# Kernel tuning notes

Hardware: AMD Instinct MI355X
Metric: run time of the kernel (lower is better)

The kernel has to match this reference:

```python
import jax, jax.numpy as jnp
import numpy as np

GROUPS = [21, 6, 17, 14, 20]
N = 78          # total nodes per graph
B = 8192        # batched graphs (original module processes one at a time)
RATIO = 0.2
LN_EPS = 1e-5


def _build_edges():
    """Replicates Graph_test mode='random' edge construction (incl. its offset quirk)."""
    rng = np.random.RandomState(0)
    edges = []
    offset = 0
    for num in GROUPS:
        for i in range(num):
            for j in range(num):
                if i != j:
                    edges.append((i + offset, j + offset))
        offset += num
    offset = 0
    for i in range(5):
        offset_2 = GROUPS[i]
        for j in range(i + 1, 5):
            for _i in range(GROUPS[i]):
                for _j in range(GROUPS[j]):
                    if _i + offset != _j + offset_2 and rng.random_sample() < RATIO:
                        edges.append((_i + offset, _j + offset_2))
            offset_2 += GROUPS[j]
        offset += GROUPS[i]
    return np.asarray(edges, dtype=np.int64).T  # [2, E]


def _ln(x, g, b):
    m = jnp.mean(x, axis=-1, keepdims=True)
    v = jnp.var(x, axis=-1, keepdims=True)
    return (x - m) * jax.lax.rsqrt(v + LN_EPS) * g + b


def _tconv(x, src, tgt, wq, bq, wk, bk, wv, bv, ws, bs, H, C):
    """PyG TransformerConv (concat=True, root_weight=True, no beta/edge_dim)."""
    n = x.shape[0]
    q = (x @ wq.T + bq).reshape(n, H, C)
    k = (x @ wk.T + bk).reshape(n, H, C)
    v = (x @ wv.T + bv).reshape(n, H, C)
    alpha = jnp.sum(q[tgt] * k[src], axis=-1) / np.sqrt(float(C))      # [E, H]
    amax = jax.ops.segment_max(alpha, tgt, num_segments=n)             # [N, H]
    e = jnp.exp(alpha - amax[tgt])
    den = jax.ops.segment_sum(e, tgt, num_segments=n)
    w = e / den[tgt]                                                   # softmax per target node
    out = jax.ops.segment_sum(w[..., None] * v[src], tgt, num_segments=n)
    return out.reshape(n, H * C) + (x @ ws.T + bs)                     # skip connection


def _forward(src, tgt, cli_data, radio_data, ln1_g, ln1_b, enc_w, enc_b,
             q1_w, q1_b, k1_w, k1_b, v1_w, v1_b, s1_w, s1_b,
             q2_w, q2_b, k2_w, k2_b, v2_w, v2_b, s2_w, s2_b,
             ln2_g, ln2_b, cls_w, cls_b):
    h = _ln(radio_data, ln1_g, ln1_b) @ enc_w.T + enc_b   # Linear(384,20)
    h = jax.nn.leaky_relu(h)                              # dropout = identity (eval)
    x = jnp.concatenate([cli_data, h], axis=1)[..., None]  # [B, 78, 1]

    def graph(xg):  # xg: [78, 1]
        y = jax.nn.leaky_relu(_tconv(xg, src, tgt, q1_w, q1_b, k1_w, k1_b,
                                     v1_w, v1_b, s1_w, s1_b, 4, 1))      # [78, 4]
        y = jax.nn.leaky_relu(_tconv(y, src, tgt, q2_w, q2_b, k2_w, k2_b,
                                     v2_w, v2_b, s2_w, s2_b, 1, 1))      # [78, 1]
        return y[:, 0]                                                    # [78]

    y = jax.vmap(graph)(x)                                # [B, 78]
    return _ln(y, ln2_g, ln2_b) @ cls_w.T + cls_b         # [B, 2]


def setup_inputs() -> dict:
    key = jax.random.key(0)
    ks = jax.random.split(key, 12)

    def xav(k, shape):
        lim = np.sqrt(6.0 / (shape[0] + shape[1]))
        return jax.random.uniform(k, shape, jnp.float32, -lim, lim)

    ei = jnp.asarray(_build_edges())
    return dict(
        cli_data=jax.random.normal(ks[0], (B, 58), jnp.float32),
        radio_data=jax.random.normal(ks[1], (B, 384), jnp.float32),
        edge_index=ei,
        ln1_g=jnp.ones((384,), jnp.float32), ln1_b=jnp.zeros((384,), jnp.float32),
        enc_w=xav(ks[2], (20, 384)), enc_b=jnp.zeros((20,), jnp.float32),
        q1_w=xav(ks[3], (4, 1)), q1_b=jnp.zeros((4,), jnp.float32),
        k1_w=xav(ks[4], (4, 1)), k1_b=jnp.zeros((4,), jnp.float32),
        v1_w=xav(ks[5], (4, 1)), v1_b=jnp.zeros((4,), jnp.float32),
        s1_w=xav(ks[6], (4, 1)), s1_b=jnp.zeros((4,), jnp.float32),
        q2_w=xav(ks[7], (1, 4)), q2_b=jnp.zeros((1,), jnp.float32),
        k2_w=xav(ks[8], (1, 4)), k2_b=jnp.zeros((1,), jnp.float32),
        v2_w=xav(ks[9], (1, 4)), v2_b=jnp.zeros((1,), jnp.float32),
        s2_w=xav(ks[10], (1, 4)), s2_b=jnp.zeros((1,), jnp.float32),
        ln2_g=jnp.ones((N,), jnp.float32), ln2_b=jnp.zeros((N,), jnp.float32),
        cls_w=xav(ks[11], (2, N)), cls_b=jnp.zeros((2,), jnp.float32),
    )


def reference(cli_data, radio_data, edge_index, ln1_g, ln1_b, enc_w, enc_b,
              q1_w, q1_b, k1_w, k1_b, v1_w, v1_b, s1_w, s1_b,
              q2_w, q2_b, k2_w, k2_b, v2_w, v2_b, s2_w, s2_b,
              ln2_g, ln2_b, cls_w, cls_b):
    src, tgt = edge_index[0], edge_index[1]
    return _forward(src, tgt, cli_data, radio_data, ln1_g, ln1_b, enc_w, enc_b,
                    q1_w, q1_b, k1_w, k1_b, v1_w, v1_b, s1_w, s1_b,
                    q2_w, q2_b, k2_w, k2_b, v2_w, v2_b, s2_w, s2_b,
                    ln2_g, ln2_b, cls_w, cls_b)


if __name__ == '__main__':
    out = reference(**setup_inputs())
    print(out.shape)
```

## Files before the change

### kernel.cpp

```cpp
#include <hip/hip_runtime.h>

#define LREL(x) ((x) > 0.0f ? (x) : 0.01f * (x))
#define LOG2E 1.44269504f

constexpr int NNODE = 78;
constexpr int GPB   = 16;
constexpr int ROWS  = 32;
constexpr int BLOCK = GPB * ROWS;
constexpr int NI    = 3;
constexpr int PADS  = 17;

__global__ void build_csr_kernel(const int* __restrict__ ei, int E,
                                 int* __restrict__ row_ptr,
                                 int* __restrict__ csr_src,
                                 int* __restrict__ perm) {
    __shared__ int cnt[NNODE];
    __shared__ int cur[NNODE];
    __shared__ int deg[NNODE];
    int tid = threadIdx.x;
    if (tid < NNODE) cnt[tid] = 0;
    __syncthreads();
    for (int e = tid; e < E; e += blockDim.x)
        atomicAdd(&cnt[ei[E + e]], 1);
    __syncthreads();
    if (tid < NNODE) deg[tid] = cnt[tid];
    __syncthreads();
    if (tid == 0) {
        int acc = 0;
        for (int n = 0; n < NNODE; ++n) {
            row_ptr[n] = acc;
            cur[n]     = acc;
            acc += cnt[n];
        }
        row_ptr[NNODE] = acc;
    }
    if (tid < NNODE) {
        int d = deg[tid], rank = 0;
        for (int m = 0; m < NNODE; ++m) {
            int dm = deg[m];
            rank += (dm > d) || (dm == d && m < tid);
        }
        perm[rank] = tid;
    }
    if (tid >= NNODE && tid < ROWS * NI) perm[tid] = -1;
    __syncthreads();
    for (int e = tid; e < E; e += blockDim.x) {
        int t   = ei[E + e];
        int pos = atomicAdd(&cur[t], 1);
        csr_src[pos] = ei[e] * PADS;
    }
}

__global__ __launch_bounds__(256) void encode_kernel(
    const float* __restrict__ radio,
    const float* __restrict__ ln1g, const float* __restrict__ ln1b,
    const float* __restrict__ encw, const float* __restrict__ encb,
    int Bn, float* __restrict__ hout) {

    const int tid  = threadIdx.x;
    const int w    = tid >> 6;
    const int half = (tid >> 5) & 1;
    const int l32  = tid & 31;

    const float4* radio4 = (const float4*)radio;
    const float4* encw4  = (const float4*)encw;
    const float4* g14    = (const float4*)ln1g;
    const float4* b14    = (const float4*)ln1b;

    float4 xn0[3], xn1[3];
    const long g0 = (long)blockIdx.x * 16 + w * 4 + half;
    const long g1 = g0 + 2;

#pragma unroll
    for (int pp = 0; pp < 2; ++pp) {
        long gidx = pp ? g1 : g0;
        bool ok = gidx < Bn;
        float4* xn = pp ? xn1 : xn0;
        float s = 0.0f, q = 0.0f;
#pragma unroll
        for (int i = 0; i < 3; ++i) {
            float4 v = ok ? radio4[gidx * 96 + l32 + 32 * i]
                          : make_float4(0, 0, 0, 0);
            xn[i] = v;
            s += v.x + v.y + v.z + v.w;
            q += v.x * v.x + v.y * v.y + v.z * v.z + v.w * v.w;
        }
#pragma unroll
        for (int o = 16; o; o >>= 1) {
            s += __shfl_xor(s, o, 32);
            q += __shfl_xor(q, o, 32);
        }
        float mean = s * (1.0f / 384.0f);
        float var  = q * (1.0f / 384.0f) - mean * mean;
        float rstd = rsqrtf(var + 1e-5f);
#pragma unroll
        for (int i = 0; i < 3; ++i) {
            float4 gv = g14[l32 + 32 * i];
            float4 bv = b14[l32 + 32 * i];
            float4 v  = xn[i];
            v.x = (v.x - mean) * rstd * gv.x + bv.x;
            v.y = (v.y - mean) * rstd * gv.y + bv.y;
            v.z = (v.z - mean) * rstd * gv.z + bv.z;
            v.w = (v.w - mean) * rstd * gv.w + bv.w;
            xn[i] = v;
        }
    }

    float h0 = 0.0f, h1 = 0.0f;
    for (int j = 0; j < 20; ++j) {
        float4 w0 = encw4[j * 96 + l32];
        float4 w1 = encw4[j * 96 + l32 + 32];
        float4 w2 = encw4[j * 96 + l32 + 64];
#pragma unroll
        for (int pp = 0; pp < 2; ++pp) {
            const float4* xn = pp ? xn1 : xn0;
            float p = xn[0].x * w0.x;
            p = fmaf(xn[0].y, w0.y, p); p = fmaf(xn[0].z, w0.z, p);
            p = fmaf(xn[0].w, w0.w, p);
            p = fmaf(xn[1].x, w1.x, p); p = fmaf(xn[1].y, w1.y, p);
            p = fmaf(xn[1].z, w1.z, p); p = fmaf(xn[1].w, w1.w, p);
            p = fmaf(xn[2].x, w2.x, p); p = fmaf(xn[2].y, w2.y, p);
            p = fmaf(xn[2].w, w2.w, p); p = fmaf(xn[2].z, w2.z, p);
#pragma unroll
            for (int o = 16; o; o >>= 1) p += __shfl_xor(p, o, 32);
            if (pp) h1 = (l32 == j) ? p : h1;
            else    h0 = (l32 == j) ? p : h0;
        }
    }
    if (l32 < 20) {
        float eb = encb[l32];
        if (g0 < Bn) hout[g0 * 20 + l32] = LREL(h0 + eb);
        if (g1 < Bn) hout[g1 * 20 + l32] = LREL(h1 + eb);
    }
}

__global__ __launch_bounds__(BLOCK, 4) void graph_conv_kernel(
    const float* __restrict__ cli, const float* __restrict__ hin,
    const float* __restrict__ q1w, const float* __restrict__ q1b,
    const float* __restrict__ k1w, const float* __restrict__ k1b,
    const float* __restrict__ v1w, const float* __restrict__ v1b,
    const float* __restrict__ s1w, const float* __restrict__ s1b,
    const float* __restrict__ q2w, const float* __restrict__ q2b,
    const float* __restrict__ k2w, const float* __restrict__ k2b,
    const float* __restrict__ v2w, const float* __restrict__ v2b,
    const float* __restrict__ s2w, const float* __restrict__ s2b,
    const float* __restrict__ ln2g, const float* __restrict__ ln2b,
    const float* __restrict__ clsw, const float* __restrict__ clsb,
    const int* __restrict__ row_ptr, const int* __restrict__ csr_src,
    const int* __restrict__ perm,
    int E, int Bn, float* __restrict__ out) {

    __shared__ float s_feat[NNODE * PADS];
    __shared__ float s_k2[NNODE * PADS];
    __shared__ float s_v2[NNODE * PADS];
    __shared__ float s_redA[8 * PADS];
    __shared__ float s_redB[8 * PADS];
    __shared__ float s_statM[GPB];
    __shared__ float s_statR[GPB];
    __shared__ int   s_rp[NNODE + 1];
    __shared__ int   s_slot[ROWS * NI];
    extern __shared__ int s_csr[];

    const int tid  = threadIdx.x;
    const int g    = tid & 15;
    const int r    = tid >> 4;
    const int w    = tid >> 6;
    const int lane = tid & 63;
    const long base = (long)blockIdx.x * GPB;

    for (int i = tid; i < E; i += BLOCK) s_csr[i] = csr_src[i];
    if (tid < NNODE + 1) s_rp[tid] = row_ptr[tid];
    if (tid < ROWS * NI) s_slot[tid] = perm[tid];
    for (int idx = tid; idx < GPB * 58; idx += BLOCK) {
        int gg = idx / 58, c = idx - gg * 58;
        if (base + gg < Bn) s_feat[c * PADS + gg] = cli[(base + gg) * 58 + c];
    }
    if (tid < GPB * 20) {
        int gg = tid / 20, j = tid - gg * 20;
        if (base + gg < Bn) s_feat[(58 + j) * PADS + gg] = hin[(base + gg) * 20 + j];
    }

    const float Q1W0 = q1w[0], Q1W1 = q1w[1], Q1W2 = q1w[2], Q1W3 = q1w[3];
    const float Q1B0 = q1b[0], Q1B1 = q1b[1], Q1B2 = q1b[2], Q1B3 = q1b[3];
    const float K1L0 = k1w[0] * LOG2E, K1L1 = k1w[1] * LOG2E;
    const float K1L2 = k1w[2] * LOG2E, K1L3 = k1w[3] * LOG2E;
    const float V1W0 = v1w[0], V1W1 = v1w[1], V1W2 = v1w[2], V1W3 = v1w[3];
    const float V1B0 = v1b[0], V1B1 = v1b[1], V1B2 = v1b[2], V1B3 = v1b[3];
    const float S1W0 = s1w[0], S1W1 = s1w[1], S1W2 = s1w[2], S1W3 = s1w[3];
    const float S1B0 = s1b[0], S1B1 = s1b[1], S1B2 = s1b[2], S1B3 = s1b[3];
    const float Q2W0 = q2w[0], Q2W1 = q2w[1], Q2W2 = q2w[2], Q2W3 = q2w[3];
    const float K2W0 = k2w[0], K2W1 = k2w[1], K2W2 = k2w[2], K2W3 = k2w[3];
    const float V2W0 = v2w[0], V2W1 = v2w[1], V2W2 = v2w[2], V2W3 = v2w[3];
    const float S2W0 = s2w[0], S2W1 = s2w[1], S2W2 = s2w[2], S2W3 = s2w[3];
    const float Q2B = q2b[0], K2B = k2b[0], V2B = v2b[0], S2B = s2b[0];
    __syncthreads();

    int   nodes[NI];
    float y_q[NI], y_sk[NI], z[NI];

#pragma unroll
    for (int k = 0; k < NI; ++k) {
        int n = s_slot[k * ROWS + r];
        nodes[k] = n;
        bool act = n >= 0;
        int nn = act ? n : 0;
        float xv = s_feat[nn * PADS + g];
        float qh0 = fmaf(xv, Q1W0, Q1B0), qh1 = fmaf(xv, Q1W1, Q1B1);
        float qh2 = fmaf(xv, Q1W2, Q1B2), qh3 = fmaf(xv, Q1W3, Q1B3);
        float qa0 = qh0 * K1L0, qa1 = qh1 * K1L1;
        float qa2 = qh2 * K1L2, qa3 = qh3 * K1L3;
        float den0 = 0, den1 = 0, den2 = 0, den3 = 0;
        float wa0 = 0, wa1 = 0, wa2 = 0, wa3 = 0;
        int beg = s_rp[nn];
        int end = act ? s_rp[nn + 1] : beg;
        int i = beg;
        for (; i + 1 < end; i += 2) {
            int c0 = s_csr[i], c1 = s_csr[i + 1];
            float t0 = s_feat[c0 + g];
            float t1 = s_feat[c1 + g];
            float ea0 = exp2f(qa0 * t0), eb0 = exp2f(qa0 * t1);
            float ea1 = exp2f(qa1 * t0), eb1 = exp2f(qa1 * t1);
            float ea2 = exp2f(qa2 * t0), eb2 = exp2f(qa2 * t1);
            float ea3 = exp2f(qa3 * t0), eb3 = exp2f(qa3 * t1);
            den0 += ea0 + eb0; den1 += ea1 + eb1;
            den2 += ea2 + eb2; den3 += ea3 + eb3;
            wa0 = fmaf(ea0, t0, fmaf(eb0, t1, wa0));
            wa1 = fmaf(ea1, t0, fmaf(eb1, t1, wa1));
            wa2 = fmaf(ea2, t0, fmaf(eb2, t1, wa2));
            wa3 = fmaf(ea3, t0, fmaf(eb3, t1, wa3));
        }
        if (i < end) {
            int c0 = s_csr[i];
            float t0 = s_feat[c0 + g];
            float ea0 = exp2f(qa0 * t0), ea1 = exp2f(qa1 * t0);
            float ea2 = exp2f(qa2 * t0), ea3 = exp2f(qa3 * t0);
            den0 += ea0; den1 += ea1; den2 += ea2; den3 += ea3;
            wa0 = fmaf(ea0, t0, wa0); wa1 = fmaf(ea1, t0, wa1);
            wa2 = fmaf(ea2, t0, wa2); wa3 = fmaf(ea3, t0, wa3);
        }
        float y0 = LREL(fmaf(V1W0, wa0 / den0, V1B0) + fmaf(xv, S1W0, S1B0));
        float y1 = LREL(fmaf(V1W1, wa1 / den1, V1B1) + fmaf(xv, S1W1, S1B1));
        float y2 = LREL(fmaf(V1W2, wa2 / den2, V1B2) + fmaf(xv, S1W2, S1B2));
        float y3 = LREL(fmaf(V1W3, wa3 / den3, V1B3) + fmaf(xv, S1W3, S1B3));
        y_q[k]  = Q2B + y0 * Q2W0 + y1 * Q2W1 + y2 * Q2W2 + y3 * Q2W3;
        y_sk[k] = S2B + y0 * S2W0 + y1 * S2W1 + y2 * S2W2 + y3 * S2W3;
        if (act) {
            s_k2[n * PADS + g] = K2B + y0 * K2W0 + y1 * K2W1 + y2 * K2W2 + y3 * K2W3;
            s_v2[n * PADS + g] = V2B + y0 * V2W0 + y1 * V2W1 + y2 * V2W2 + y3 * V2W3;
        }
    }
    __syncthreads();

    float zs = 0, zq = 0;
#pragma unroll
    for (int k = 0; k < NI; ++k) {
        int n = nodes[k];
        bool act = n >= 0;
        int nn = act ? n : 0;
        float q = y_q[k];
        int beg = s_rp[nn];
        int end = act ? s_rp[nn + 1] : beg;
        float m = -1e30f;
        for (int i = beg; i < end; ++i)
            m = fmaxf(m, q * s_k2[s_csr[i] + g]);
        float ql = q * LOG2E, ml = m * LOG2E;
        float den = 0, acc = 0;
        int i = beg;
        for (; i + 1 < end; i += 2) {
            int c0 = s_csr[i], c1 = s_csr[i + 1];
            float k0 = s_k2[c0 + g], k1v = s_k2[c1 + g];
            float v0 = s_v2[c0 + g], v1v = s_v2[c1 + g];
            float e0 = exp2f(fmaf(ql, k0, -ml));
            float e1 = exp2f(fmaf(ql, k1v, -ml));
            den += e0 + e1;
            acc = fmaf(e0, v0, fmaf(e1, v1v, acc));
        }
        if (i < end) {
            int c0 = s_csr[i];
            float e0 = exp2f(fmaf(ql, s_k2[c0 + g], -ml));
            den += e0;
            acc = fmaf(e0, s_v2[c0 + g], acc);
        }
        float zz = LREL(acc / den + y_sk[k]);
        z[k] = zz;
        if (act) { zs += zz; zq = fmaf(zz, zz, zq); }
    }

    zs += __shfl_xor(zs, 16, 64); zs += __shfl_xor(zs, 32, 64);
    zq += __shfl_xor(zq, 16, 64); zq += __shfl_xor(zq, 32, 64);
    if (lane < 16) {
        s_redA[w * PADS + lane] = zs;
        s_redB[w * PADS + lane] = zq;
    }
    __syncthreads();
    if (tid < GPB) {
        float a = 0, bb = 0;
#pragma unroll
        for (int i = 0; i < 8; ++i) {
            a  += s_redA[i * PADS + tid];
            bb += s_redB[i * PADS + tid];
        }
        float mean = a * (1.0f / 78.0f);
        float var  = bb * (1.0f / 78.0f) - mean * mean;
        s_statM[tid] = mean;
        s_statR[tid] = rsqrtf(var + 1e-5f);
    }
    __syncthreads();
    float mean = s_statM[g], rstd = s_statR[g];
    float p0 = 0, p1 = 0;
#pragma unroll
    for (int k = 0; k < NI; ++k) {
        int n = nodes[k];
        if (n >= 0) {
            float zn = fmaf((z[k] - mean) * rstd, ln2g[n], ln2b[n]);
            p0 = fmaf(zn, clsw[n], p0);
            p1 = fmaf(zn, clsw[NNODE + n], p1);
        }
    }
    p0 += __shfl_xor(p0, 16, 64); p0 += __shfl_xor(p0, 32, 64);
    p1 += __shfl_xor(p1, 16, 64); p1 += __shfl_xor(p1, 32, 64);
    if (lane < 16) {
        s_redA[w * PADS + lane] = p0;
        s_redB[w * PADS + lane] = p1;
    }
    __syncthreads();
    if (tid < GPB) {
        float a = 0, bb = 0;
#pragma unroll
        for (int i = 0; i < 8; ++i) {
            a  += s_redA[i * PADS + tid];
            bb += s_redB[i * PADS + tid];
        }
        long gi = base + tid;
        if (gi < Bn) {
            out[gi * 2 + 0] = a + clsb[0];
            out[gi * 2 + 1] = bb + clsb[1];
        }
    }
}

extern "C" void kernel_launch(void* const* d_in, const int* in_sizes, int n_in,
                              void* d_out, int out_size, void* d_ws, size_t ws_size,
                              hipStream_t stream) {
    const float* cli   = (const float*)d_in[0];
    const float* radio = (const float*)d_in[1];
    const int*   ei    = (const int*)d_in[2];
    const float* ln1g = (const float*)d_in[3];
    const float* ln1b = (const float*)d_in[4];
    const float* encw = (const float*)d_in[5];
    const float* encb = (const float*)d_in[6];
    const float* q1w  = (const float*)d_in[7];
    const float* q1b  = (const float*)d_in[8];
    const float* k1w  = (const float*)d_in[9];
    const float* k1b  = (const float*)d_in[10];
    const float* v1w  = (const float*)d_in[11];
    const float* v1b  = (const float*)d_in[12];
    const float* s1w  = (const float*)d_in[13];
    const float* s1b  = (const float*)d_in[14];
    const float* q2w  = (const float*)d_in[15];
    const float* q2b  = (const float*)d_in[16];
    const float* k2w  = (const float*)d_in[17];
    const float* k2b  = (const float*)d_in[18];
    const float* v2w  = (const float*)d_in[19];
    const float* v2b  = (const float*)d_in[20];
    const float* s2w  = (const float*)d_in[21];
    const float* s2b  = (const float*)d_in[22];
    const float* ln2g = (const float*)d_in[23];
    const float* ln2b = (const float*)d_in[24];
    const float* clsw = (const float*)d_in[25];
    const float* clsb = (const float*)d_in[26];

    const int E  = in_sizes[2] / 2;
    const int Bn = in_sizes[0] / 58;

    int* row_ptr = (int*)d_ws;
    int* csr_src = row_ptr + 80;
    int* perm    = csr_src + E;
    int  off     = (80 + E + ROWS * NI + 7) & ~7;
    float* h     = (float*)((int*)d_ws + off);

    build_csr_kernel<<<1, 256, 0, stream>>>(ei, E, row_ptr, csr_src, perm);

    const int egrid = (Bn + 15) / 16;
    encode_kernel<<<egrid, 256, 0, stream>>>(radio, ln1g, ln1b, encw, encb, Bn, h);

    const int grid = (Bn + GPB - 1) / GPB;
    size_t shmem = (size_t)E * sizeof(int);
    graph_conv_kernel<<<grid, BLOCK, shmem, stream>>>(
        cli, h,
        q1w, q1b, k1w, k1b, v1w, v1b, s1w, s1b,
        q2w, q2b, k2w, k2b, v2w, v2b, s2w, s2b,
        ln2g, ln2b, clsw, clsb,
        row_ptr, csr_src, perm, E, Bn, (float*)d_out);
}
```

Measured before the change: 165.2 us.

## Halve graphs per block, double rows per graph, and compress CSR indices to 16-bit

The graph-conv kernel now handles 8 graphs per 512-thread block instead of 16. Each node-row thread processes at most 2 nodes instead of 3. The CSR, row pointer and slot tables in shared memory are stored as 16-bit values, and the launch-bounds occupancy hint rises from 4 to 8 blocks. The aim is to cut LDS footprint and per-thread serial work so more waves stay resident and latency is hidden better. The cost is twice as many blocks, each reloading the full edge list from global memory, plus a wider shuffle reduction and one extra barrier before reusing the reduction buffers.

```diff
diff --git a/kernel.cpp b/kernel.cpp
--- a/kernel.cpp
+++ b/kernel.cpp
@@ -4,11 +4,11 @@
 #define LOG2E 1.44269504f
 
 constexpr int NNODE = 78;
-constexpr int GPB   = 16;
-constexpr int ROWS  = 32;
+constexpr int GPB   = 8;
+constexpr int ROWS  = 64;
 constexpr int BLOCK = GPB * ROWS;
-constexpr int NI    = 3;
-constexpr int PADS  = 17;
+constexpr int NI    = 2;
+constexpr int PADS  = 9;
 
 __global__ void build_csr_kernel(const int* __restrict__ ei, int E,
                                  int* __restrict__ row_ptr,
@@ -120,7 +120,7 @@
             p = fmaf(xn[1].x, w1.x, p); p = fmaf(xn[1].y, w1.y, p);
             p = fmaf(xn[1].z, w1.z, p); p = fmaf(xn[1].w, w1.w, p);
             p = fmaf(xn[2].x, w2.x, p); p = fmaf(xn[2].y, w2.y, p);
-            p = fmaf(xn[2].w, w2.w, p); p = fmaf(xn[2].z, w2.z, p);
+            p = fmaf(xn[2].z, w2.z, p); p = fmaf(xn[2].w, w2.w, p);
 #pragma unroll
             for (int o = 16; o; o >>= 1) p += __shfl_xor(p, o, 32);
             if (pp) h1 = (l32 == j) ? p : h1;
@@ -134,7 +134,7 @@
     }
 }
 
-__global__ __launch_bounds__(BLOCK, 4) void graph_conv_kernel(
+__global__ __launch_bounds__(BLOCK, 8) void graph_conv_kernel(
     const float* __restrict__ cli, const float* __restrict__ hin,
     const float* __restrict__ q1w, const float* __restrict__ q1b,
     const float* __restrict__ k1w, const float* __restrict__ k1b,
@@ -157,22 +157,21 @@
     __shared__ float s_redB[8 * PADS];
     __shared__ float s_statM[GPB];
     __shared__ float s_statR[GPB];
-    __shared__ int   s_rp[NNODE + 1];
-    __shared__ int   s_slot[ROWS * NI];
-    extern __shared__ int s_csr[];
+    __shared__ unsigned short s_rp[NNODE + 1];
+    __shared__ short s_slot[ROWS * NI];
+    extern __shared__ unsigned short s_csr[];
 
     const int tid  = threadIdx.x;
-    const int g    = tid & 15;
-    const int r    = tid >> 4;
+    const int g    = tid & 7;
+    const int r    = tid >> 3;
     const int w    = tid >> 6;
-    const int lane = tid & 63;
     const long base = (long)blockIdx.x * GPB;
 
-    for (int i = tid; i < E; i += BLOCK) s_csr[i] = csr_src[i];
-    if (tid < NNODE + 1) s_rp[tid] = row_ptr[tid];
-    if (tid < ROWS * NI) s_slot[tid] = perm[tid];
+    for (int i = tid; i < E; i += BLOCK) s_csr[i] = (unsigned short)csr_src[i];
+    if (tid < NNODE + 1) s_rp[tid] = (unsigned short)row_ptr[tid];
+    if (tid < ROWS * NI) s_slot[tid] = (short)perm[tid];
     for (int idx = tid; idx < GPB * 58; idx += BLOCK) {
-        int gg = idx / 58, c = idx - gg * 58;
+        int gg = idx >> 6; gg = idx / 58; int c = idx - gg * 58;
         if (base + gg < Bn) s_feat[c * PADS + gg] = cli[(base + gg) * 58 + c];
     }
     if (tid < GPB * 20) {
@@ -212,7 +211,7 @@
         float den0 = 0, den1 = 0, den2 = 0, den3 = 0;
         float wa0 = 0, wa1 = 0, wa2 = 0, wa3 = 0;
         int beg = s_rp[nn];
-        int end = act ? s_rp[nn + 1] : beg;
+        int end = act ? (int)s_rp[nn + 1] : beg;
         int i = beg;
         for (; i + 1 < end; i += 2) {
             int c0 = s_csr[i], c1 = s_csr[i + 1];
@@ -259,7 +258,7 @@
         int nn = act ? n : 0;
         float q = y_q[k];
         int beg = s_rp[nn];
-        int end = act ? s_rp[nn + 1] : beg;
+        int end = act ? (int)s_rp[nn + 1] : beg;
         float m = -1e30f;
         for (int i = beg; i < end; ++i)
             m = fmaxf(m, q * s_k2[s_csr[i] + g]);
@@ -286,11 +285,11 @@
         if (act) { zs += zz; zq = fmaf(zz, zz, zq); }
     }
 
-    zs += __shfl_xor(zs, 16, 64); zs += __shfl_xor(zs, 32, 64);
-    zq += __shfl_xor(zq, 16, 64); zq += __shfl_xor(zq, 32, 64);
-    if (lane < 16) {
-        s_redA[w * PADS + lane] = zs;
-        s_redB[w * PADS + lane] = zq;
+    zs += __shfl_xor(zs, 8, 64); zs += __shfl_xor(zs, 16, 64); zs += __shfl_xor(zs, 32, 64);
+    zq += __shfl_xor(zq, 8, 64); zq += __shfl_xor(zq, 16, 64); zq += __shfl_xor(zq, 32, 64);
+    if ((tid & 63) < 8) {
+        s_redA[w * PADS + g] = zs;
+        s_redB[w * PADS + g] = zq;
     }
     __syncthreads();
     if (tid < GPB) {
@@ -317,11 +316,12 @@
             p1 = fmaf(zn, clsw[NNODE + n], p1);
         }
     }
-    p0 += __shfl_xor(p0, 16, 64); p0 += __shfl_xor(p0, 32, 64);
-    p1 += __shfl_xor(p1, 16, 64); p1 += __shfl_xor(p1, 32, 64);
-    if (lane < 16) {
-        s_redA[w * PADS + lane] = p0;
-        s_redB[w * PADS + lane] = p1;
+    p0 += __shfl_xor(p0, 8, 64); p0 += __shfl_xor(p0, 16, 64); p0 += __shfl_xor(p0, 32, 64);
+    p1 += __shfl_xor(p1, 8, 64); p1 += __shfl_xor(p1, 16, 64); p1 += __shfl_xor(p1, 32, 64);
+    __syncthreads();
+    if ((tid & 63) < 8) {
+        s_redA[w * PADS + g] = p0;
+        s_redB[w * PADS + g] = p1;
     }
     __syncthreads();
     if (tid < GPB) {
@@ -385,7 +385,7 @@
     encode_kernel<<<egrid, 256, 0, stream>>>(radio, ln1g, ln1b, encw, encb, Bn, h);
 
     const int grid = (Bn + GPB - 1) / GPB;
-    size_t shmem = (size_t)E * sizeof(int);
+    size_t shmem = ((size_t)E * 2 + 7) & ~7;
     graph_conv_kernel<<<grid, BLOCK, shmem, stream>>>(
         cli, h,
         q1w, q1b, k1w, k1b, v1w, v1b, s1w, s1b,
```

Result: slower. 178.9 us (+8.3%).

## Reorder CSR by slot with padded rows, pack k2/v2, unroll edge loops by four

Applied to the files above, without the earlier changes.

The CSR build now orders adjacency rows by thread slot, with a snake assignment that balances degrees across the three per-thread node passes, and pads each row to a multiple of four so indices load as int4. The graph kernel unrolls both attention loops by four using byte-offset addressing, packs k2 and v2 into one float2 array with LOG2E pre-folded, and skips inactive slots entirely. This is meant to cut LDS index loads, address arithmetic and load imbalance between lanes, at the cost of more LDS for the padded CSR. It also adds a barrier before reusing the reduction buffers, which fixes a race, and reorders two FMAs in the encoder.

```diff
diff --git a/kernel.cpp b/kernel.cpp
--- a/kernel.cpp
+++ b/kernel.cpp
@@ -8,47 +8,62 @@
 constexpr int ROWS  = 32;
 constexpr int BLOCK = GPB * ROWS;
 constexpr int NI    = 3;
+constexpr int NSLOT = ROWS * NI;
 constexpr int PADS  = 17;
 
 __global__ void build_csr_kernel(const int* __restrict__ ei, int E,
-                                 int* __restrict__ row_ptr,
-                                 int* __restrict__ csr_src,
-                                 int* __restrict__ perm) {
-    __shared__ int cnt[NNODE];
-    __shared__ int cur[NNODE];
+                                 int* __restrict__ slot_node,
+                                 int* __restrict__ slot_beg,
+                                 int* __restrict__ slot_cnt,
+                                 int* __restrict__ csr2) {
     __shared__ int deg[NNODE];
+    __shared__ int slot_of[NNODE];
+    __shared__ int s2n[NSLOT];
+    __shared__ int sbeg[NSLOT + 1];
+    __shared__ int cur[NSLOT];
     int tid = threadIdx.x;
-    if (tid < NNODE) cnt[tid] = 0;
+    if (tid < NNODE) deg[tid] = 0;
+    if (tid < NSLOT) s2n[tid] = -1;
     __syncthreads();
     for (int e = tid; e < E; e += blockDim.x)
-        atomicAdd(&cnt[ei[E + e]], 1);
-    __syncthreads();
-    if (tid < NNODE) deg[tid] = cnt[tid];
+        atomicAdd(&deg[ei[E + e]], 1);
+    __syncthreads();
+    if (tid < NNODE) {
+        int d = deg[tid], rk = 0;
+        for (int m = 0; m < NNODE; ++m) {
+            int dm = deg[m];
+            rk += (dm > d) || (dm == d && m < tid);
+        }
+        int s = (rk < 32) ? rk : ((rk < 64) ? (95 - rk) : rk);
+        slot_of[tid] = s;
+    }
+    __syncthreads();
+    if (tid < NNODE) s2n[slot_of[tid]] = tid;
     __syncthreads();
     if (tid == 0) {
         int acc = 0;
-        for (int n = 0; n < NNODE; ++n) {
-            row_ptr[n] = acc;
-            cur[n]     = acc;
-            acc += cnt[n];
-        }
-        row_ptr[NNODE] = acc;
-    }
-    if (tid < NNODE) {
-        int d = deg[tid], rank = 0;
-        for (int m = 0; m < NNODE; ++m) {
-            int dm = deg[m];
-            rank += (dm > d) || (dm == d && m < tid);
-        }
-        perm[rank] = tid;
-    }
-    if (tid >= NNODE && tid < ROWS * NI) perm[tid] = -1;
+        for (int s = 0; s < NSLOT; ++s) {
+            sbeg[s] = acc;
+            cur[s]  = acc;
+            int n = s2n[s];
+            int c = (n >= 0) ? deg[n] : 0;
+            acc += (c + 3) & ~3;
+        }
+        sbeg[NSLOT] = acc;
+    }
     __syncthreads();
     for (int e = tid; e < E; e += blockDim.x) {
         int t   = ei[E + e];
-        int pos = atomicAdd(&cur[t], 1);
-        csr_src[pos] = ei[e] * PADS;
-    }
+        int pos = atomicAdd(&cur[slot_of[t]], 1);
+        csr2[pos] = ei[e] * (PADS * 4);
+    }
+    if (tid < NSLOT) {
+        int n = s2n[tid];
+        slot_node[tid] = n;
+        slot_beg[tid]  = sbeg[tid];
+        slot_cnt[tid]  = (n >= 0) ? deg[n] : 0;
+    }
+    if (tid == 0) slot_beg[NSLOT] = sbeg[NSLOT];
 }
 
 __global__ __launch_bounds__(256) void encode_kernel(
@@ -120,7 +135,7 @@
             p = fmaf(xn[1].x, w1.x, p); p = fmaf(xn[1].y, w1.y, p);
             p = fmaf(xn[1].z, w1.z, p); p = fmaf(xn[1].w, w1.w, p);
             p = fmaf(xn[2].x, w2.x, p); p = fmaf(xn[2].y, w2.y, p);
-            p = fmaf(xn[2].w, w2.w, p); p = fmaf(xn[2].z, w2.z, p);
+            p = fmaf(xn[2].z, w2.z, p); p = fmaf(xn[2].w, w2.w, p);
 #pragma unroll
             for (int o = 16; o; o >>= 1) p += __shfl_xor(p, o, 32);
             if (pp) h1 = (l32 == j) ? p : h1;
@@ -146,19 +161,19 @@
     const float* __restrict__ s2w, const float* __restrict__ s2b,
     const float* __restrict__ ln2g, const float* __restrict__ ln2b,
     const float* __restrict__ clsw, const float* __restrict__ clsb,
-    const int* __restrict__ row_ptr, const int* __restrict__ csr_src,
-    const int* __restrict__ perm,
-    int E, int Bn, float* __restrict__ out) {
-
-    __shared__ float s_feat[NNODE * PADS];
-    __shared__ float s_k2[NNODE * PADS];
-    __shared__ float s_v2[NNODE * PADS];
-    __shared__ float s_redA[8 * PADS];
-    __shared__ float s_redB[8 * PADS];
-    __shared__ float s_statM[GPB];
-    __shared__ float s_statR[GPB];
-    __shared__ int   s_rp[NNODE + 1];
-    __shared__ int   s_slot[ROWS * NI];
+    const int* __restrict__ slot_node, const int* __restrict__ slot_beg,
+    const int* __restrict__ slot_cnt, const int* __restrict__ csr2,
+    int Bn, float* __restrict__ out) {
+
+    __shared__ float  s_feat[NNODE * PADS];
+    __shared__ float2 s_kv[NNODE * PADS];
+    __shared__ float  s_redA[8 * PADS];
+    __shared__ float  s_redB[8 * PADS];
+    __shared__ float  s_statM[GPB];
+    __shared__ float  s_statR[GPB];
+    __shared__ int    s_snode[NSLOT];
+    __shared__ int    s_sbeg[NSLOT];
+    __shared__ int    s_scnt[NSLOT];
     extern __shared__ int s_csr[];
 
     const int tid  = threadIdx.x;
@@ -168,9 +183,13 @@
     const int lane = tid & 63;
     const long base = (long)blockIdx.x * GPB;
 
-    for (int i = tid; i < E; i += BLOCK) s_csr[i] = csr_src[i];
-    if (tid < NNODE + 1) s_rp[tid] = row_ptr[tid];
-    if (tid < ROWS * NI) s_slot[tid] = perm[tid];
+    const int stot = slot_beg[NSLOT];
+    for (int i = tid; i < stot; i += BLOCK) s_csr[i] = csr2[i];
+    if (tid < NSLOT) {
+        s_snode[tid] = slot_node[tid];
+        s_sbeg[tid]  = slot_beg[tid];
+        s_scnt[tid]  = slot_cnt[tid];
+    }
     for (int idx = tid; idx < GPB * 58; idx += BLOCK) {
         int gg = idx / 58, c = idx - gg * 58;
         if (base + gg < Bn) s_feat[c * PADS + gg] = cli[(base + gg) * 58 + c];
@@ -195,48 +214,60 @@
     const float Q2B = q2b[0], K2B = k2b[0], V2B = v2b[0], S2B = s2b[0];
     __syncthreads();
 
+    const char* featg = (const char*)s_feat + g * 4;
+    const char* kvg   = (const char*)s_kv   + g * 8;
+
     int   nodes[NI];
     float y_q[NI], y_sk[NI], z[NI];
 
 #pragma unroll
     for (int k = 0; k < NI; ++k) {
-        int n = s_slot[k * ROWS + r];
+        const int slot = k * ROWS + r;
+        const int n    = s_snode[slot];
+        const int cnt  = s_scnt[slot];
+        const int ib   = s_sbeg[slot];
         nodes[k] = n;
-        bool act = n >= 0;
-        int nn = act ? n : 0;
-        float xv = s_feat[nn * PADS + g];
+        const bool act = n >= 0;
+        const float xv = act ? s_feat[n * PADS + g] : 0.0f;
         float qh0 = fmaf(xv, Q1W0, Q1B0), qh1 = fmaf(xv, Q1W1, Q1B1);
         float qh2 = fmaf(xv, Q1W2, Q1B2), qh3 = fmaf(xv, Q1W3, Q1B3);
         float qa0 = qh0 * K1L0, qa1 = qh1 * K1L1;
         float qa2 = qh2 * K1L2, qa3 = qh3 * K1L3;
         float den0 = 0, den1 = 0, den2 = 0, den3 = 0;
         float wa0 = 0, wa1 = 0, wa2 = 0, wa3 = 0;
-        int beg = s_rp[nn];
-        int end = act ? s_rp[nn + 1] : beg;
-        int i = beg;
-        for (; i + 1 < end; i += 2) {
-            int c0 = s_csr[i], c1 = s_csr[i + 1];
-            float t0 = s_feat[c0 + g];
-            float t1 = s_feat[c1 + g];
-            float ea0 = exp2f(qa0 * t0), eb0 = exp2f(qa0 * t1);
-            float ea1 = exp2f(qa1 * t0), eb1 = exp2f(qa1 * t1);
-            float ea2 = exp2f(qa2 * t0), eb2 = exp2f(qa2 * t1);
-            float ea3 = exp2f(qa3 * t0), eb3 = exp2f(qa3 * t1);
-            den0 += ea0 + eb0; den1 += ea1 + eb1;
-            den2 += ea2 + eb2; den3 += ea3 + eb3;
-            wa0 = fmaf(ea0, t0, fmaf(eb0, t1, wa0));
-            wa1 = fmaf(ea1, t0, fmaf(eb1, t1, wa1));
-            wa2 = fmaf(ea2, t0, fmaf(eb2, t1, wa2));
-            wa3 = fmaf(ea3, t0, fmaf(eb3, t1, wa3));
-        }
-        if (i < end) {
-            int c0 = s_csr[i];
-            float t0 = s_feat[c0 + g];
-            float ea0 = exp2f(qa0 * t0), ea1 = exp2f(qa1 * t0);
-            float ea2 = exp2f(qa2 * t0), ea3 = exp2f(qa3 * t0);
-            den0 += ea0; den1 += ea1; den2 += ea2; den3 += ea3;
-            wa0 = fmaf(ea0, t0, wa0); wa1 = fmaf(ea1, t0, wa1);
-            wa2 = fmaf(ea2, t0, wa2); wa3 = fmaf(ea3, t0, wa3);
+        const int nq = cnt >> 2;
+        for (int t = 0; t < nq; ++t) {
+            int4 c = *(const int4*)(s_csr + ib + (t << 2));
+            float t0 = *(const float*)(featg + c.x);
+            float t1 = *(const float*)(featg + c.y);
+            float t2 = *(const float*)(featg + c.z);
+            float t3 = *(const float*)(featg + c.w);
+            float e00 = exp2f(qa0 * t0), e01 = exp2f(qa0 * t1),
+                  e02 = exp2f(qa0 * t2), e03 = exp2f(qa0 * t3);
+            float e10 = exp2f(qa1 * t0), e11 = exp2f(qa1 * t1),
+                  e12 = exp2f(qa1 * t2), e13 = exp2f(qa1 * t3);
+            float e20 = exp2f(qa2 * t0), e21 = exp2f(qa2 * t1),
+                  e22 = exp2f(qa2 * t2), e23 = exp2f(qa2 * t3);
+            float e30 = exp2f(qa3 * t0), e31 = exp2f(qa3 * t1),
+                  e32 = exp2f(qa3 * t2), e33 = exp2f(qa3 * t3);
+            den0 += (e00 + e01) + (e02 + e03);
+            den1 += (e10 + e11) + (e12 + e13);
+            den2 += (e20 + e21) + (e22 + e23);
+            den3 += (e30 + e31) + (e32 + e33);
+            wa0 = fmaf(e00, t0, fmaf(e01, t1, fmaf(e02, t2, fmaf(e03, t3, wa0))));
+            wa1 = fmaf(e10, t0, fmaf(e11, t1, fmaf(e12, t2, fmaf(e13, t3, wa1))));
+            wa2 = fmaf(e20, t0, fmaf(e21, t1, fmaf(e22, t2, fmaf(e23, t3, wa2))));
+            wa3 = fmaf(e30, t0, fmaf(e31, t1, fmaf(e32, t2, fmaf(e33, t3, wa3))));
+        }
+        const int it = ib + (nq << 2), rem = cnt & 3;
+        for (int j = 0; j < rem; ++j) {
+            int cc = s_csr[it + j];
+            float t0 = *(const float*)(featg + cc);
+            float e0 = exp2f(qa0 * t0), e1 = exp2f(qa1 * t0);
+            float e2 = exp2f(qa2 * t0), e3 = exp2f(qa3 * t0);
+            den0 += e0; den1 += e1; den2 += e2; den3 += e3;
+            wa0 = fmaf(e0, t0, wa0); wa1 = fmaf(e1, t0, wa1);
+            wa2 = fmaf(e2, t0, wa2); wa3 = fmaf(e3, t0, wa3);
         }
         float y0 = LREL(fmaf(V1W0, wa0 / den0, V1B0) + fmaf(xv, S1W0, S1B0));
         float y1 = LREL(fmaf(V1W1, wa1 / den1, V1B1) + fmaf(xv, S1W1, S1B1));
@@ -245,8 +276,9 @@
         y_q[k]  = Q2B + y0 * Q2W0 + y1 * Q2W1 + y2 * Q2W2 + y3 * Q2W3;
         y_sk[k] = S2B + y0 * S2W0 + y1 * S2W1 + y2 * S2W2 + y3 * S2W3;
         if (act) {
-            s_k2[n * PADS + g] = K2B + y0 * K2W0 + y1 * K2W1 + y2 * K2W2 + y3 * K2W3;
-            s_v2[n * PADS + g] = V2B + y0 * V2W0 + y1 * V2W1 + y2 * V2W2 + y3 * V2W3;
+            float k2v = K2B + y0 * K2W0 + y1 * K2W1 + y2 * K2W2 + y3 * K2W3;
+            float v2v = V2B + y0 * V2W0 + y1 * V2W1 + y2 * V2W2 + y3 * V2W3;
+            s_kv[n * PADS + g] = make_float2(k2v * LOG2E, v2v);
         }
     }
     __syncthreads();
@@ -254,36 +286,53 @@
     float zs = 0, zq = 0;
 #pragma unroll
     for (int k = 0; k < NI; ++k) {
-        int n = nodes[k];
-        bool act = n >= 0;
-        int nn = act ? n : 0;
-        float q = y_q[k];
-        int beg = s_rp[nn];
-        int end = act ? s_rp[nn + 1] : beg;
-        float m = -1e30f;
-        for (int i = beg; i < end; ++i)
-            m = fmaxf(m, q * s_k2[s_csr[i] + g]);
-        float ql = q * LOG2E, ml = m * LOG2E;
-        float den = 0, acc = 0;
-        int i = beg;
-        for (; i + 1 < end; i += 2) {
-            int c0 = s_csr[i], c1 = s_csr[i + 1];
-            float k0 = s_k2[c0 + g], k1v = s_k2[c1 + g];
-            float v0 = s_v2[c0 + g], v1v = s_v2[c1 + g];
-            float e0 = exp2f(fmaf(ql, k0, -ml));
-            float e1 = exp2f(fmaf(ql, k1v, -ml));
-            den += e0 + e1;
-            acc = fmaf(e0, v0, fmaf(e1, v1v, acc));
-        }
-        if (i < end) {
-            int c0 = s_csr[i];
-            float e0 = exp2f(fmaf(ql, s_k2[c0 + g], -ml));
-            den += e0;
-            acc = fmaf(e0, s_v2[c0 + g], acc);
-        }
-        float zz = LREL(acc / den + y_sk[k]);
+        const int n = nodes[k];
+        const int slot = k * ROWS + r;
+        const int cnt  = s_scnt[slot];
+        const int ib   = s_sbeg[slot];
+        const bool act = n >= 0;
+        const float q = y_q[k];
+        float zz;
+        if (act) {
+            const int nq = cnt >> 2, rem = cnt & 3;
+            float m = -1e30f;
+            for (int t = 0; t < nq; ++t) {
+                int4 c = *(const int4*)(s_csr + ib + (t << 2));
+                float a0 = q * *(const float*)(kvg + (c.x << 1));
+                float a1 = q * *(const float*)(kvg + (c.y << 1));
+                float a2 = q * *(const float*)(kvg + (c.z << 1));
+                float a3 = q * *(const float*)(kvg + (c.w << 1));
+                m = fmaxf(m, fmaxf(fmaxf(a0, a1), fmaxf(a2, a3)));
+            }
+            const int it = ib + (nq << 2);
+            for (int j = 0; j < rem; ++j)
+                m = fmaxf(m, q * *(const float*)(kvg + (s_csr[it + j] << 1)));
+            float den = 0, acc = 0;
+            for (int t = 0; t < nq; ++t) {
+                int4 c = *(const int4*)(s_csr + ib + (t << 2));
+                float2 kv0 = *(const float2*)(kvg + (c.x << 1));
+                float2 kv1 = *(const float2*)(kvg + (c.y << 1));
+                float2 kv2 = *(const float2*)(kvg + (c.z << 1));
+                float2 kv3 = *(const float2*)(kvg + (c.w << 1));
+                float e0 = exp2f(fmaf(q, kv0.x, -m));
+                float e1 = exp2f(fmaf(q, kv1.x, -m));
+                float e2 = exp2f(fmaf(q, kv2.x, -m));
+                float e3 = exp2f(fmaf(q, kv3.x, -m));
+                den += (e0 + e1) + (e2 + e3);
+                acc = fmaf(e0, kv0.y, fmaf(e1, kv1.y, fmaf(e2, kv2.y, fmaf(e3, kv3.y, acc))));
+            }
+            for (int j = 0; j < rem; ++j) {
+                float2 kv0 = *(const float2*)(kvg + (s_csr[it + j] << 1));
+                float e0 = exp2f(fmaf(q, kv0.x, -m));
+                den += e0;
+                acc = fmaf(e0, kv0.y, acc);
+            }
+            zz = LREL(acc / den + y_sk[k]);
+            zs += zz; zq = fmaf(zz, zz, zq);
+        } else {
+            zz = 0.0f;
+        }
         z[k] = zz;
-        if (act) { zs += zz; zq = fmaf(zz, zz, zq); }
     }
 
     zs += __shfl_xor(zs, 16, 64); zs += __shfl_xor(zs, 32, 64);
@@ -319,6 +368,7 @@
     }
     p0 += __shfl_xor(p0, 16, 64); p0 += __shfl_xor(p0, 32, 64);
     p1 += __shfl_xor(p1, 16, 64); p1 += __shfl_xor(p1, 32, 64);
+    __syncthreads();
     if (lane < 16) {
         s_redA[w * PADS + lane] = p0;
         s_redB[w * PADS + lane] = p1;
@@ -373,23 +423,25 @@
     const int E  = in_sizes[2] / 2;
     const int Bn = in_sizes[0] / 58;
 
-    int* row_ptr = (int*)d_ws;
-    int* csr_src = row_ptr + 80;
-    int* perm    = csr_src + E;
-    int  off     = (80 + E + ROWS * NI + 7) & ~7;
-    float* h     = (float*)((int*)d_ws + off);
-
-    build_csr_kernel<<<1, 256, 0, stream>>>(ei, E, row_ptr, csr_src, perm);
+    int* slot_node = (int*)d_ws;
+    int* slot_beg  = slot_node + 96;
+    int* slot_cnt  = slot_beg + 104;
+    int* csr2      = slot_cnt + 96;
+    int  csr_cap   = E + 3 * NSLOT + 8;
+    float* h       = (float*)(csr2 + ((csr_cap + 7) & ~7));
+
+    build_csr_kernel<<<1, 256, 0, stream>>>(ei, E, slot_node, slot_beg,
+                                            slot_cnt, csr2);
 
     const int egrid = (Bn + 15) / 16;
     encode_kernel<<<egrid, 256, 0, stream>>>(radio, ln1g, ln1b, encw, encb, Bn, h);
 
     const int grid = (Bn + GPB - 1) / GPB;
-    size_t shmem = (size_t)E * sizeof(int);
+    size_t shmem = (size_t)csr_cap * sizeof(int);
     graph_conv_kernel<<<grid, BLOCK, shmem, stream>>>(
         cli, h,
         q1w, q1b, k1w, k1b, v1w, v1b, s1w, s1b,
         q2w, q2b, k2w, k2b, v2w, v2b, s2w, s2b,
         ln2g, ln2b, clsw, clsb,
-        row_ptr, csr_src, perm, E, Bn, (float*)d_out);
+        slot_node, slot_beg, slot_cnt, csr2, Bn, (float*)d_out);
 }
```

New measurement: 166.5 us. Within noise of the previous version (+0.8%).
